# Kernel tuning notes

Measured on AMD Instinct MI355X. Metric: run time of the kernel, lower is better.

Reference implementation:

```python
import math
import jax, jax.numpy as jnp
import numpy as np

B, N, D = 4, 4096, 1024
H, M = 16, 64
HD = D // H  # 64
EPS = 1e-6


def favor_features(data, proj):
    # data: [B,H,N,hd], proj: [M,hd] -> [B,H,N,M]
    hd = data.shape[-1]
    m = proj.shape[0]
    dn = data / math.sqrt(hd)
    norm_sq = 0.5 * jnp.sum(dn * dn, axis=-1, keepdims=True)  # [B,H,N,1]
    comb = jnp.einsum('bhnd,md->bhnm', dn, proj) - norm_sq
    comb = comb - jnp.max(comb, axis=-1, keepdims=True)
    return jnp.exp(comb) / math.sqrt(m) + EPS


def setup_inputs() -> dict:
    key = jax.random.key(0)
    ks = jax.random.split(key, 6)
    x = jax.random.normal(ks[0], (B, N, D), dtype=jnp.float32)
    qkv_w = jax.random.normal(ks[1], (3 * D, D), dtype=jnp.float32) * (1.0 / math.sqrt(D))
    qkv_b = jnp.zeros((3 * D,), dtype=jnp.float32)
    proj_w = jax.random.normal(ks[2], (D, D), dtype=jnp.float32) * (1.0 / math.sqrt(D))
    proj_b = jnp.zeros((D,), dtype=jnp.float32)
    pm = jax.random.normal(ks[3], (M, HD), dtype=jnp.float32)
    pm = pm / jnp.linalg.norm(pm, axis=-1, keepdims=True)
    return {"x": x, "qkv_w": qkv_w, "qkv_b": qkv_b, "proj_w": proj_w,
            "proj_b": proj_b, "projection_matrix": pm}


def reference(x, qkv_w, qkv_b, proj_w, proj_b, projection_matrix):
    b, n, d = x.shape
    qkv = x @ qkv_w.T + qkv_b                      # [B,N,3D]
    qkv = qkv.reshape(b, n, 3, H, HD)
    qkv = jnp.transpose(qkv, (2, 0, 3, 1, 4))      # [3,B,H,N,hd]
    q, k, v = qkv[0], qkv[1], qkv[2]
    q_p = favor_features(q, projection_matrix)     # [B,H,N,M]
    k_p = favor_features(k, projection_matrix)     # [B,H,N,M]
    kv = jnp.einsum('bhnm,bhnv->bhmv', k_p, v)     # [B,H,M,hd]
    out = jnp.einsum('bhnm,bhmv->bhnv', q_p, kv)   # [B,H,N,hd]
    k_sum = jnp.sum(k_p, axis=2)                   # [B,H,M]
    normalizer = jnp.einsum('bhnm,bhm->bhn', q_p, k_sum)[..., None]
    out = out / (normalizer + EPS)
    out = jnp.transpose(out, (0, 2, 1, 3)).reshape(b, n, d)
    return out @ proj_w.T + proj_b
```

## Files before the change

kernel.cpp:

```cpp
#include <hip/hip_runtime.h>
#include <math.h>

#define B_  4
#define N_  4096
#define D_  1024
#define H_  16
#define HD_ 64
#define M_  64
#define TD_ 3072
#define EPS_ 1e-6f

typedef __attribute__((ext_vector_type(8))) short short8;
typedef __attribute__((ext_vector_type(4))) float floatx4;
typedef unsigned int uint32;
typedef unsigned short ushort;

__device__ __forceinline__ void cvt2(float f0, float f1, uint32& hp, uint32& lp)
{
    uint32 b0 = __float_as_uint(f0), b1 = __float_as_uint(f1);
    hp = (b1 & 0xFFFF0000u) | (b0 >> 16);
    float l0 = f0 - __uint_as_float(b0 & 0xFFFF0000u);
    float l1 = f1 - __uint_as_float(b1 & 0xFFFF0000u);
    lp = (__float_as_uint(l1) & 0xFFFF0000u) | (__float_as_uint(l0) >> 16);
}

__global__ __launch_bounds__(256) void split_kernel(
    const float* __restrict__ src, ushort* __restrict__ hi,
    ushort* __restrict__ lo, int n)
{
    size_t i = ((size_t)blockIdx.x * 256 + threadIdx.x) * 8;
    if (i >= (size_t)n) return;
    float4 f0 = *(const float4*)(src + i);
    float4 f1 = *(const float4*)(src + i + 4);
    uint4 h, l;
    cvt2(f0.x, f0.y, h.x, l.x); cvt2(f0.z, f0.w, h.y, l.y);
    cvt2(f1.x, f1.y, h.z, l.z); cvt2(f1.z, f1.w, h.w, l.w);
    *(uint4*)(hi + i) = h;
    *(uint4*)(lo + i) = l;
}

#define LDSTR 40

__global__ __launch_bounds__(256, 2) void gemm_presplit_nt_bias(
    const ushort* __restrict__ Ah, const ushort* __restrict__ Al,
    const ushort* __restrict__ Bh, const ushort* __restrict__ Bl,
    const float* __restrict__ bias, float* __restrict__ C,
    int Nx, int Kx)
{
    __shared__ __align__(16) ushort AhiS[128*LDSTR], AloS[128*LDSTR];
    __shared__ __align__(16) ushort BhiS[128*LDSTR], BloS[128*LDSTR];

    const int t    = threadIdx.x;
    const int bm   = blockIdx.y * 128, bn = blockIdx.x * 128;
    const int lane = t & 63, wave = t >> 6;
    const int wm   = wave >> 1, wn = wave & 1;
    const int l16  = lane & 15, quad = lane >> 4;
    const int r    = t >> 1;
    const int ko   = (t & 1) * 16;

    floatx4 acc[4][4];
#pragma unroll
    for (int i = 0; i < 4; i++)
#pragma unroll
        for (int j = 0; j < 4; j++) acc[i][j] = (floatx4)0.f;

    const ushort* aph = Ah + (size_t)(bm + r) * Kx + ko;
    const ushort* apl = Al + (size_t)(bm + r) * Kx + ko;
    const ushort* bph = Bh + (size_t)(bn + r) * Kx + ko;
    const ushort* bpl = Bl + (size_t)(bn + r) * Kx + ko;

    for (int k0 = 0; k0 < Kx; k0 += 32) {
        uint4 vah0 = *(const uint4*)(aph + k0);
        uint4 vah1 = *(const uint4*)(aph + k0 + 8);
        uint4 val0 = *(const uint4*)(apl + k0);
        uint4 val1 = *(const uint4*)(apl + k0 + 8);
        uint4 vbh0 = *(const uint4*)(bph + k0);
        uint4 vbh1 = *(const uint4*)(bph + k0 + 8);
        uint4 vbl0 = *(const uint4*)(bpl + k0);
        uint4 vbl1 = *(const uint4*)(bpl + k0 + 8);

        __syncthreads();

        *(uint4*)&AhiS[r*LDSTR + ko]     = vah0;
        *(uint4*)&AhiS[r*LDSTR + ko + 8] = vah1;
        *(uint4*)&AloS[r*LDSTR + ko]     = val0;
        *(uint4*)&AloS[r*LDSTR + ko + 8] = val1;
        *(uint4*)&BhiS[r*LDSTR + ko]     = vbh0;
        *(uint4*)&BhiS[r*LDSTR + ko + 8] = vbh1;
        *(uint4*)&BloS[r*LDSTR + ko]     = vbl0;
        *(uint4*)&BloS[r*LDSTR + ko + 8] = vbl1;

        __syncthreads();

        short8 ah[4], al[4], bh[4], bl[4];
#pragma unroll
        for (int mi = 0; mi < 4; mi++) {
            int row = (wm*64 + mi*16 + l16) * LDSTR + quad*8;
            ah[mi] = *(const short8*)&AhiS[row];
            al[mi] = *(const short8*)&AloS[row];
        }
#pragma unroll
        for (int ni = 0; ni < 4; ni++) {
            int row = (wn*64 + ni*16 + l16) * LDSTR + quad*8;
            bh[ni] = *(const short8*)&BhiS[row];
            bl[ni] = *(const short8*)&BloS[row];
        }
#pragma unroll
        for (int mi = 0; mi < 4; mi++)
#pragma unroll
            for (int ni = 0; ni < 4; ni++) {
                floatx4 d = acc[mi][ni];
                d = __builtin_amdgcn_mfma_f32_16x16x32_bf16(ah[mi], bh[ni], d, 0, 0, 0);
                d = __builtin_amdgcn_mfma_f32_16x16x32_bf16(al[mi], bh[ni], d, 0, 0, 0);
                d = __builtin_amdgcn_mfma_f32_16x16x32_bf16(ah[mi], bl[ni], d, 0, 0, 0);
                acc[mi][ni] = d;
            }
    }

    float bia[4];
#pragma unroll
    for (int ni = 0; ni < 4; ni++)
        bia[ni] = bias[bn + wn*64 + ni*16 + l16];
#pragma unroll
    for (int mi = 0; mi < 4; mi++)
#pragma unroll
        for (int rr = 0; rr < 4; rr++) {
            int row = bm + wm*64 + mi*16 + quad*4 + rr;
            float* crow = C + (size_t)row * Nx + bn + wn*64 + l16;
#pragma unroll
            for (int ni = 0; ni < 4; ni++)
                crow[ni*16] = acc[mi][ni][rr] + bia[ni];
        }
}

__device__ __forceinline__ void gload16(const void* g, void* l)
{
    __builtin_amdgcn_global_load_lds(
        (const __attribute__((address_space(1))) unsigned int*)g,
        (__attribute__((address_space(3))) unsigned int*)l,
        16, 0, 0);
}

#define BAR() asm volatile("s_barrier" ::: "memory")

__global__ __launch_bounds__(512, 2) void gemm256_pipe(
    const ushort* __restrict__ Ah, const ushort* __restrict__ Al,
    const ushort* __restrict__ Bh, const ushort* __restrict__ Bl,
    const float* __restrict__ bias, float* __restrict__ C,
    int Nx, int Kx)
{
    __shared__ __align__(16) ushort lds[65536];

    const int t    = threadIdx.x;
    const int wave = t >> 6, lane = t & 63;
    const int wm   = wave >> 2, wn = wave & 3;
    const int l16  = lane & 15, quad = lane >> 4;

    const int gx  = gridDim.x;
    const int nwg = gx * gridDim.y;
    int bid = blockIdx.y * gx + blockIdx.x;
    const int cpx = nwg >> 3;
    bid = (bid & 7) * cpx + (bid >> 3);
    const int bm = (bid / gx) * 256;
    const int bn = (bid % gx) * 256;

    const int r0   = t >> 2;
    const int cswz = ((((t & 3) << 4) ^ ((t & 0x18) << 1)) >> 1);
    const size_t aOff = (size_t)(bm + r0) * Kx + cswz;
    const size_t bOff = (size_t)(bn + r0) * Kx + cswz;

    const int ucol = (quad * 8) ^ ((l16 & 6) << 2);
    const int aRB  = (wm * 64 + l16) * 32 + ucol;
    const int bRB  = (wn * 32 + l16) * 32 + ucol;

    floatx4 acc[8][4];
#pragma unroll
    for (int i = 0; i < 8; i++)
#pragma unroll
        for (int j = 0; j < 4; j++) acc[i][j] = (floatx4)0.f;

#define STAGE_A2(NB, KT) do {                                                 \
    size_t g0_ = (size_t)(KT) * 32;                                           \
    gload16(Ah + aOff + g0_,                   &lds[(NB) + wave*512]);        \
    gload16(Al + aOff + g0_,                   &lds[(NB) + 8192 + wave*512]); \
    gload16(Ah + aOff + (size_t)128*Kx + g0_,  &lds[(NB) + 4096 + wave*512]); \
    gload16(Al + aOff + (size_t)128*Kx + g0_,  &lds[(NB) + 12288 + wave*512]);\
} while (0)
#define STAGE_B2(NB, KT) do {                                                 \
    size_t g0_ = (size_t)(KT) * 32;                                           \
    gload16(Bh + bOff + g0_,                   &lds[(NB) + 16384 + wave*512]);\
    gload16(Bl + bOff + g0_,                   &lds[(NB) + 24576 + wave*512]);\
    gload16(Bh + bOff + (size_t)128*Kx + g0_,  &lds[(NB) + 20480 + wave*512]);\
    gload16(Bl + bOff + (size_t)128*Kx + g0_,  &lds[(NB) + 28672 + wave*512]);\
} while (0)

    const int NT = Kx >> 5;

    STAGE_A2(0, 0);
    STAGE_B2(0, 0);
    asm volatile("s_waitcnt vmcnt(0)" ::: "memory");
    BAR();

    for (int kt = 0; kt < NT; kt++) {
        const int cb  = (kt & 1) << 15;
        const int nb  = cb ^ 32768;
        const int ktn = (kt + 1 < NT) ? kt + 1 : NT - 1;

        short8 ah_[4], al_[4], bh_[4], bl_[4];
        const int aB0 = cb + aRB;
        const int bB0 = cb + 16384 + bRB;

        STAGE_A2(nb, ktn);

#pragma unroll
        for (int g = 0; g < 4; g++) {
            bh_[g] = *(const short8*)&lds[bB0 + (g >> 1)*4096 + (g & 1)*512];
            bl_[g] = *(const short8*)&lds[bB0 + 8192 + (g >> 1)*4096 + (g & 1)*512];
        }
#pragma unroll
        for (int mi = 0; mi < 4; mi++) {
            ah_[mi] = *(const short8*)&lds[aB0 + mi*512];
            al_[mi] = *(const short8*)&lds[aB0 + 8192 + mi*512];
        }
        asm volatile("s_waitcnt lgkmcnt(0)" ::: "memory");
        __builtin_amdgcn_sched_barrier(0);
        __builtin_amdgcn_s_setprio(1);
#pragma unroll
        for (int mi = 0; mi < 4; mi++)
#pragma unroll
            for (int g = 0; g < 4; g++) {
                floatx4 d = acc[mi][g];
                d = __builtin_amdgcn_mfma_f32_16x16x32_bf16(ah_[mi], bh_[g], d, 0, 0, 0);
                d = __builtin_amdgcn_mfma_f32_16x16x32_bf16(al_[mi], bh_[g], d, 0, 0, 0);
                d = __builtin_amdgcn_mfma_f32_16x16x32_bf16(ah_[mi], bl_[g], d, 0, 0, 0);
                acc[mi][g] = d;
            }
        __builtin_amdgcn_s_setprio(0);
        __builtin_amdgcn_sched_barrier(0);

        STAGE_B2(nb, ktn);
#pragma unroll
        for (int mi = 0; mi < 4; mi++) {
            ah_[mi] = *(const short8*)&lds[aB0 + 4096 + mi*512];
            al_[mi] = *(const short8*)&lds[aB0 + 12288 + mi*512];
        }
        asm volatile("s_waitcnt lgkmcnt(0)" ::: "memory");
        __builtin_amdgcn_sched_barrier(0);
        __builtin_amdgcn_s_setprio(1);
#pragma unroll
        for (int mi = 0; mi < 4; mi++)
#pragma unroll
            for (int g = 0; g < 4; g++) {
                floatx4 d = acc[4 + mi][g];
                d = __builtin_amdgcn_mfma_f32_16x16x32_bf16(ah_[mi], bh_[g], d, 0, 0, 0);
                d = __builtin_amdgcn_mfma_f32_16x16x32_bf16(al_[mi], bh_[g], d, 0, 0, 0);
                d = __builtin_amdgcn_mfma_f32_16x16x32_bf16(ah_[mi], bl_[g], d, 0, 0, 0);
                acc[4 + mi][g] = d;
            }
        __builtin_amdgcn_s_setprio(0);
        __builtin_amdgcn_sched_barrier(0);

        asm volatile("s_waitcnt vmcnt(0)" ::: "memory");
        BAR();
    }

#pragma unroll
    for (int f = 0; f < 8; f++) {
        const int row = bm + (f >> 2)*128 + wm*64 + (f & 3)*16 + quad*4;
#pragma unroll
        for (int g = 0; g < 4; g++) {
            const int col = bn + (g >> 1)*128 + wn*32 + (g & 1)*16 + l16;
            const float bb = bias[col];
#pragma unroll
            for (int rr = 0; rr < 4; rr++)
                C[(size_t)(row + rr) * Nx + col] = acc[f][g][rr] + bb;
        }
    }
#undef STAGE_A2
#undef STAGE_B2
}

__global__ __launch_bounds__(256) void favor_features_kernel(
    const float* __restrict__ qkvb, const float* __restrict__ proj,
    float* __restrict__ qp, float* __restrict__ kp)
{
    __shared__ float  projT[64*64];
    __shared__ float4 dnbuf[4][64];
    const int t = threadIdx.x;
    const int wave = t >> 6, lane = t & 63;
    const int part = blockIdx.y;
    float* outp = (part == 0) ? qp : kp;

    for (int i = t; i < 4096; i += 256)
        projT[(i & 63) * 64 + (i >> 6)] = proj[i];
    __syncthreads();

    const int h = blockIdx.x >> 6;
    const int n0 = (blockIdx.x & 63) * 64;
    const float* src = qkvb + part * D_ + h * HD_ + lane;

    for (int iter = 0; iter < 4; iter++) {
        const int n = n0 + iter * 16 + wave * 4;
        float v0 = src[(size_t)(n+0) * TD_];
        float v1 = src[(size_t)(n+1) * TD_];
        float v2 = src[(size_t)(n+2) * TD_];
        float v3 = src[(size_t)(n+3) * TD_];
        float4 dn = make_float4(v0*0.125f, v1*0.125f, v2*0.125f, v3*0.125f);
        dnbuf[wave][lane] = dn;
        float s0 = dn.x*dn.x, s1 = dn.y*dn.y, s2 = dn.z*dn.z, s3 = dn.w*dn.w;
#pragma unroll
        for (int off = 32; off >= 1; off >>= 1) {
            s0 += __shfl_xor(s0, off, 64);
            s1 += __shfl_xor(s1, off, 64);
            s2 += __shfl_xor(s2, off, 64);
            s3 += __shfl_xor(s3, off, 64);
        }
        float c0 = -0.5f*s0, c1 = -0.5f*s1, c2 = -0.5f*s2, c3 = -0.5f*s3;
#pragma unroll
        for (int d = 0; d < 64; d++) {
            float p = projT[d*64 + lane];
            float4 q = dnbuf[wave][d];
            c0 = fmaf(q.x, p, c0);
            c1 = fmaf(q.y, p, c1);
            c2 = fmaf(q.z, p, c2);
            c3 = fmaf(q.w, p, c3);
        }
        float m0 = c0, m1 = c1, m2 = c2, m3 = c3;
#pragma unroll
        for (int off = 32; off >= 1; off >>= 1) {
            m0 = fmaxf(m0, __shfl_xor(m0, off, 64));
            m1 = fmaxf(m1, __shfl_xor(m1, off, 64));
            m2 = fmaxf(m2, __shfl_xor(m2, off, 64));
            m3 = fmaxf(m3, __shfl_xor(m3, off, 64));
        }
        float r0 = expf(c0 - m0) * 0.125f + EPS_;
        float r1 = expf(c1 - m1) * 0.125f + EPS_;
        float r2 = expf(c2 - m2) * 0.125f + EPS_;
        float r3 = expf(c3 - m3) * 0.125f + EPS_;
        size_t orow = ((size_t)h * N_ + n) * 64 + lane;
        outp[orow]       = r0;
        outp[orow + 64]  = r1;
        outp[orow + 128] = r2;
        outp[orow + 192] = r3;
    }
}

__global__ __launch_bounds__(256) void kv_partial_kernel(
    const float* __restrict__ qkvb, const float* __restrict__ kp,
    float* __restrict__ kvpart, float* __restrict__ kspart)
{
    const int t = threadIdx.x;
    const int h = blockIdx.x;
    const int c = blockIdx.y;
    const int n0 = c * 128;
    const int m0 = (t & 15) * 4;
    const int v0 = (t >> 4) * 4;

    const float* kpsrc = kp + ((size_t)h * N_ + n0) * 64 + m0;
    const float* vsrc  = qkvb + (size_t)n0 * TD_ + 2 * D_ + h * HD_ + v0;

    float acc[4][4];
#pragma unroll
    for (int i = 0; i < 4; i++)
#pragma unroll
        for (int j = 0; j < 4; j++) acc[i][j] = 0.f;
    float ks[4] = {0.f, 0.f, 0.f, 0.f};

#pragma unroll 4
    for (int n = 0; n < 128; n++) {
        float4 kq = *(const float4*)(kpsrc + (size_t)n * 64);
        float4 vq = *(const float4*)(vsrc  + (size_t)n * TD_);
        acc[0][0] = fmaf(kq.x, vq.x, acc[0][0]);
        acc[0][1] = fmaf(kq.x, vq.y, acc[0][1]);
        acc[0][2] = fmaf(kq.x, vq.z, acc[0][2]);
        acc[0][3] = fmaf(kq.x, vq.w, acc[0][3]);
        acc[1][0] = fmaf(kq.y, vq.x, acc[1][0]);
        acc[1][1] = fmaf(kq.y, vq.y, acc[1][1]);
        acc[1][2] = fmaf(kq.y, vq.z, acc[1][2]);
        acc[1][3] = fmaf(kq.y, vq.w, acc[1][3]);
        acc[2][0] = fmaf(kq.z, vq.x, acc[2][0]);
        acc[2][1] = fmaf(kq.z, vq.y, acc[2][1]);
        acc[2][2] = fmaf(kq.z, vq.z, acc[2][2]);
        acc[2][3] = fmaf(kq.z, vq.w, acc[2][3]);
        acc[3][0] = fmaf(kq.w, vq.x, acc[3][0]);
        acc[3][1] = fmaf(kq.w, vq.y, acc[3][1]);
        acc[3][2] = fmaf(kq.w, vq.z, acc[3][2]);
        acc[3][3] = fmaf(kq.w, vq.w, acc[3][3]);
        if (v0 == 0) {
            ks[0] += kq.x; ks[1] += kq.y; ks[2] += kq.z; ks[3] += kq.w;
        }
    }

    float* kvp = kvpart + (((size_t)h * 32 + c) * 4096) + m0 * 64 + v0;
#pragma unroll
    for (int i = 0; i < 4; i++)
        *(float4*)(kvp + i * 64) = make_float4(acc[i][0], acc[i][1], acc[i][2], acc[i][3]);

    if (v0 == 0) {
        float* ksp = kspart + ((size_t)h * 32 + c) * 64 + m0;
        *(float4*)ksp = make_float4(ks[0], ks[1], ks[2], ks[3]);
    }
}

__global__ __launch_bounds__(256) void kv_reduce_kernel(
    const float* __restrict__ kvpart, const float* __restrict__ kspart,
    float* __restrict__ kv, float* __restrict__ ksum)
{
    const int t = threadIdx.x;
    const int h = blockIdx.x;
    const int e0 = t * 16;

    float4 s[4];
#pragma unroll
    for (int i = 0; i < 4; i++) s[i] = make_float4(0.f, 0.f, 0.f, 0.f);
    float kss = 0.f;

    for (int c = 0; c < 32; c++) {
        const float* p = kvpart + (((size_t)h * 32 + c) * 4096) + e0;
#pragma unroll
        for (int i = 0; i < 4; i++) {
            float4 x = *(const float4*)(p + i * 4);
            s[i].x += x.x; s[i].y += x.y; s[i].z += x.z; s[i].w += x.w;
        }
        if (t < 64) kss += kspart[((size_t)h * 32 + c) * 64 + t];
    }

    float* kvo = kv + (size_t)h * 4096 + e0;
#pragma unroll
    for (int i = 0; i < 4; i++) *(float4*)(kvo + i * 4) = s[i];
    if (t < 64) ksum[h * 64 + t] = kss;
}

__global__ __launch_bounds__(256) void out_kernel(
    const float* __restrict__ qp, const float* __restrict__ kv,
    const float* __restrict__ ksum, ushort* __restrict__ attn_hi,
    ushort* __restrict__ attn_lo)
{
    __shared__ float  kvs[4096];
    __shared__ float  kss[64];
    __shared__ float4 qbuf[4][64];
    const int t = threadIdx.x, lane = t & 63, wave = t >> 6;
    const int h = blockIdx.x;
    const int n0 = blockIdx.y * 64;

    for (int i = t; i < 4096; i += 256) kvs[i] = kv[(size_t)h * 4096 + i];
    if (t < 64) kss[t] = ksum[h * 64 + t];
    __syncthreads();

    const float* qsrc = qp + (size_t)h * N_ * 64 + lane;
    const size_t dbase = h * HD_ + lane;

    for (int iter = 0; iter < 4; iter++) {
        const int n = n0 + iter * 16 + wave * 4;
        float q0 = qsrc[(size_t)(n+0) * 64];
        float q1 = qsrc[(size_t)(n+1) * 64];
        float q2 = qsrc[(size_t)(n+2) * 64];
        float q3 = qsrc[(size_t)(n+3) * 64];
        qbuf[wave][lane] = make_float4(q0, q1, q2, q3);
        float t0 = q0 * kss[lane], t1 = q1 * kss[lane];
        float t2 = q2 * kss[lane], t3 = q3 * kss[lane];
#pragma unroll
        for (int off = 32; off >= 1; off >>= 1) {
            t0 += __shfl_xor(t0, off, 64);
            t1 += __shfl_xor(t1, off, 64);
            t2 += __shfl_xor(t2, off, 64);
            t3 += __shfl_xor(t3, off, 64);
        }
        float a0 = 0.f, a1 = 0.f, a2 = 0.f, a3 = 0.f;
#pragma unroll
        for (int m = 0; m < 64; m++) {
            float kvv = kvs[m*64 + lane];
            float4 q = qbuf[wave][m];
            a0 = fmaf(q.x, kvv, a0);
            a1 = fmaf(q.y, kvv, a1);
            a2 = fmaf(q.z, kvv, a2);
            a3 = fmaf(q.w, kvv, a3);
        }
        float r[4];
        r[0] = a0 / (t0 + EPS_); r[1] = a1 / (t1 + EPS_);
        r[2] = a2 / (t2 + EPS_); r[3] = a3 / (t3 + EPS_);
#pragma unroll
        for (int i = 0; i < 4; i++) {
            uint32 bits = __float_as_uint(r[i]);
            float lof = r[i] - __uint_as_float(bits & 0xFFFF0000u);
            size_t idx = (size_t)(n + i) * D_ + dbase;
            attn_hi[idx] = (ushort)(bits >> 16);
            attn_lo[idx] = (ushort)(__float_as_uint(lof) >> 16);
        }
    }
}

extern "C" void kernel_launch(void* const* d_in, const int* in_sizes, int n_in,
                              void* d_out, int out_size, void* d_ws, size_t ws_size,
                              hipStream_t stream)
{
    const float* x      = (const float*)d_in[0];
    const float* qkv_w  = (const float*)d_in[1];
    const float* qkv_b  = (const float*)d_in[2];
    const float* proj_w = (const float*)d_in[3];
    const float* proj_b = (const float*)d_in[4];
    const float* pm     = (const float*)d_in[5];
    float* out = (float*)d_out;
    float* ws  = (float*)d_ws;

    const bool tierA = ws_size >= 327553024ULL;
    const bool tierB = ws_size >= 176558080ULL;

    if (tierA) {
        float* qkvbA  = ws;
        float* qp     = qkvbA + 50331648;
        float* kp     = qp + 4194304;
        float* kvb    = kp + 4194304;
        float* ksum   = kvb + 65536;
        float* kvpart = ksum + 1024;
        float* kspart = kvpart + 2097152;
        float* axw    = kspart + 32768;
        float* wsplit = axw + 16777216;

        ushort* xw_hi    = (ushort*)axw;
        ushort* xw_lo    = xw_hi + 16777216;
        ushort* attn_hi  = xw_hi;
        ushort* attn_lo  = xw_lo;
        ushort* qkvw_hi  = (ushort*)wsplit;
        ushort* qkvw_lo  = qkvw_hi + 3145728;
        ushort* projw_hi = qkvw_lo + 3145728;
        ushort* projw_lo = projw_hi + 1048576;

        split_kernel<<<1536, 256, 0, stream>>>(qkv_w, qkvw_hi, qkvw_lo, TD_*D_);
        split_kernel<<<512,  256, 0, stream>>>(proj_w, projw_hi, projw_lo, D_*D_);
        split_kernel<<<8192, 256, 0, stream>>>(x, xw_hi, xw_lo, B_*N_*D_);

        gemm256_pipe<<<dim3(12, 64), 512, 0, stream>>>(
            xw_hi, xw_lo, qkvw_hi, qkvw_lo, qkv_b, qkvbA, TD_, D_);

        for (int b = 0; b < B_; b++) {
            const float* qkvb = qkvbA + (size_t)b * N_ * TD_;
            dim3 g2(1024, 2);
            favor_features_kernel<<<g2, 256, 0, stream>>>(qkvb, pm, qp, kp);
            dim3 g3(16, 32);
            kv_partial_kernel<<<g3, 256, 0, stream>>>(qkvb, kp, kvpart, kspart);
            kv_reduce_kernel<<<16, 256, 0, stream>>>(kvpart, kspart, kvb, ksum);
            dim3 g4(16, 64);
            out_kernel<<<g4, 256, 0, stream>>>(qp, kvb, ksum,
                attn_hi + (size_t)b * N_ * D_, attn_lo + (size_t)b * N_ * D_);
        }

        gemm256_pipe<<<dim3(4, 64), 512, 0, stream>>>(
            attn_hi, attn_lo, projw_hi, projw_lo, proj_b, out, D_, D_);
    } else if (tierB) {
        float* qkvb   = ws;
        float* qp     = ws + 12582912;
        float* kp     = qp + 4194304;
        float* kvb    = kp + 4194304;
        float* ksum   = kvb + 65536;
        float* kvpart = ksum + 1024;
        float* kspart = kvpart + 2097152;
        float* wsplit = kspart + 32768;
        float* attnA  = wsplit + 4194304;

        ushort* xw_hi    = (ushort*)qp;
        ushort* xw_lo    = xw_hi + 4194304;
        ushort* qkvw_hi  = (ushort*)wsplit;
        ushort* qkvw_lo  = qkvw_hi + 3145728;
        ushort* projw_hi = qkvw_lo + 3145728;
        ushort* projw_lo = projw_hi + 1048576;
        ushort* attnA_hi = (ushort*)attnA;
        ushort* attnA_lo = attnA_hi + 16777216;

        split_kernel<<<1536, 256, 0, stream>>>(qkv_w, qkvw_hi, qkvw_lo, TD_*D_);
        split_kernel<<<512,  256, 0, stream>>>(proj_w, projw_hi, projw_lo, D_*D_);

        for (int b = 0; b < B_; b++) {
            const float* xb = x + (size_t)b * N_ * D_;
            split_kernel<<<2048, 256, 0, stream>>>(xb, xw_hi, xw_lo, N_*D_);
            gemm256_pipe<<<dim3(12, 16), 512, 0, stream>>>(
                xw_hi, xw_lo, qkvw_hi, qkvw_lo, qkv_b, qkvb, TD_, D_);
            dim3 g2(1024, 2);
            favor_features_kernel<<<g2, 256, 0, stream>>>(qkvb, pm, qp, kp);
            dim3 g3(16, 32);
            kv_partial_kernel<<<g3, 256, 0, stream>>>(qkvb, kp, kvpart, kspart);
            kv_reduce_kernel<<<16, 256, 0, stream>>>(kvpart, kspart, kvb, ksum);
            dim3 g4(16, 64);
            out_kernel<<<g4, 256, 0, stream>>>(qp, kvb, ksum,
                attnA_hi + (size_t)b * N_ * D_, attnA_lo + (size_t)b * N_ * D_);
        }

        gemm256_pipe<<<dim3(4, 64), 512, 0, stream>>>(
            attnA_hi, attnA_lo, projw_hi, projw_lo, proj_b, out, D_, D_);
    } else {
        float* qkvb   = ws;
        float* qpreg  = ws + 12582912;
        float* kpreg  = qpreg + 4194304;
        float* kvb    = kpreg + 4194304;
        float* ksum   = kvb + 65536;
        float* kvpart = ksum + 1024;
        float* kspart = kvpart + 2097152;
        float* wsplit = kspart + 32768;

        ushort* xw_hi   = (ushort*)qpreg;
        ushort* xw_lo   = xw_hi + 4194304;
        float*  qp      = qpreg;
        float*  kp      = kpreg;
        ushort* attn_hi = (ushort*)kpreg;
        ushort* attn_lo = attn_hi + 4194304;
        ushort* qkvw_hi = (ushort*)wsplit;
        ushort* qkvw_lo = qkvw_hi + 3145728;
        ushort* projw_hi= qkvw_lo + 3145728;
        ushort* projw_lo= projw_hi + 1048576;

        split_kernel<<<TD_*D_/2048, 256, 0, stream>>>(qkv_w, qkvw_hi, qkvw_lo, TD_*D_);
        split_kernel<<<D_*D_/2048,  256, 0, stream>>>(proj_w, projw_hi, projw_lo, D_*D_);

        for (int b = 0; b < B_; b++) {
            const float* xb = x + (size_t)b * N_ * D_;
            float* outb = out + (size_t)b * N_ * D_;

            split_kernel<<<N_*D_/2048, 256, 0, stream>>>(xb, xw_hi, xw_lo, N_*D_);

            gemm256_pipe<<<dim3(12, 16), 512, 0, stream>>>(
                xw_hi, xw_lo, qkvw_hi, qkvw_lo, qkv_b, qkvb, TD_, D_);

            dim3 g2(1024, 2);
            favor_features_kernel<<<g2, 256, 0, stream>>>(qkvb, pm, qp, kp);

            dim3 g3(16, 32);
            kv_partial_kernel<<<g3, 256, 0, stream>>>(qkvb, kp, kvpart, kspart);
            kv_reduce_kernel<<<16, 256, 0, stream>>>(kvpart, kspart, kvb, ksum);

            dim3 g4(16, 64);
            out_kernel<<<g4, 256, 0, stream>>>(qp, kvb, ksum, attn_hi, attn_lo);

            dim3 g5(D_ / 128, N_ / 128);
            gemm_presplit_nt_bias<<<g5, 256, 0, stream>>>(
                attn_hi, attn_lo, projw_hi, projw_lo, proj_b, outb, D_, D_);
        }
    }
}
```

Before: 965.0 us.

## Issue both GEMM stage loads early and widen kv_reduce grid

In the pipelined GEMM main loop, the B-tile prefetch is now issued together with the A-tile prefetch at the top of each iteration. The explicit lgkmcnt waits and sched_barriers around the MFMA blocks are removed, leaving the compiler to schedule LDS reads and MFMAs. Separately, kv_reduce is split across 4x more blocks, each thread summing one float4 instead of four, to raise parallelism in a tiny kernel. Removing the manual waits and barriers risks worse instruction interleaving or extra register pressure.

```diff
diff --git a/kernel.cpp b/kernel.cpp
--- a/kernel.cpp
+++ b/kernel.cpp
@@ -141,7 +141,7 @@
         16, 0, 0);
 }
 
-#define BAR() asm volatile("s_barrier" ::: "memory")
+#define BAR()  asm volatile("s_barrier" ::: "memory")
 
 __global__ __launch_bounds__(512, 2) void gemm256_pipe(
     const ushort* __restrict__ Ah, const ushort* __restrict__ Al,
@@ -211,6 +211,7 @@
         const int bB0 = cb + 16384 + bRB;
 
         STAGE_A2(nb, ktn);
+        STAGE_B2(nb, ktn);
 
 #pragma unroll
         for (int g = 0; g < 4; g++) {
@@ -222,8 +223,6 @@
             ah_[mi] = *(const short8*)&lds[aB0 + mi*512];
             al_[mi] = *(const short8*)&lds[aB0 + 8192 + mi*512];
         }
-        asm volatile("s_waitcnt lgkmcnt(0)" ::: "memory");
-        __builtin_amdgcn_sched_barrier(0);
         __builtin_amdgcn_s_setprio(1);
 #pragma unroll
         for (int mi = 0; mi < 4; mi++)
@@ -236,16 +235,12 @@
                 acc[mi][g] = d;
             }
         __builtin_amdgcn_s_setprio(0);
-        __builtin_amdgcn_sched_barrier(0);
-
-        STAGE_B2(nb, ktn);
+
 #pragma unroll
         for (int mi = 0; mi < 4; mi++) {
             ah_[mi] = *(const short8*)&lds[aB0 + 4096 + mi*512];
             al_[mi] = *(const short8*)&lds[aB0 + 12288 + mi*512];
         }
-        asm volatile("s_waitcnt lgkmcnt(0)" ::: "memory");
-        __builtin_amdgcn_sched_barrier(0);
         __builtin_amdgcn_s_setprio(1);
 #pragma unroll
         for (int mi = 0; mi < 4; mi++)
@@ -258,7 +253,6 @@
                 acc[4 + mi][g] = d;
             }
         __builtin_amdgcn_s_setprio(0);
-        __builtin_amdgcn_sched_barrier(0);
 
         asm volatile("s_waitcnt vmcnt(0)" ::: "memory");
         BAR();
@@ -408,27 +402,20 @@
 {
     const int t = threadIdx.x;
     const int h = blockIdx.x;
-    const int e0 = t * 16;
-
-    float4 s[4];
-#pragma unroll
-    for (int i = 0; i < 4; i++) s[i] = make_float4(0.f, 0.f, 0.f, 0.f);
+    const int e0 = (blockIdx.y * 256 + t) * 4;
+
+    float4 s = make_float4(0.f, 0.f, 0.f, 0.f);
     float kss = 0.f;
+    const bool doks = (blockIdx.y == 0) && (t < 64);
 
     for (int c = 0; c < 32; c++) {
-        const float* p = kvpart + (((size_t)h * 32 + c) * 4096) + e0;
-#pragma unroll
-        for (int i = 0; i < 4; i++) {
-            float4 x = *(const float4*)(p + i * 4);
-            s[i].x += x.x; s[i].y += x.y; s[i].z += x.z; s[i].w += x.w;
-        }
-        if (t < 64) kss += kspart[((size_t)h * 32 + c) * 64 + t];
-    }
-
-    float* kvo = kv + (size_t)h * 4096 + e0;
-#pragma unroll
-    for (int i = 0; i < 4; i++) *(float4*)(kvo + i * 4) = s[i];
-    if (t < 64) ksum[h * 64 + t] = kss;
+        float4 x = *(const float4*)(kvpart + (((size_t)h * 32 + c) * 4096) + e0);
+        s.x += x.x; s.y += x.y; s.z += x.z; s.w += x.w;
+        if (doks) kss += kspart[((size_t)h * 32 + c) * 64 + t];
+    }
+
+    *(float4*)(kv + (size_t)h * 4096 + e0) = s;
+    if (doks) ksum[h * 64 + t] = kss;
 }
 
 __global__ __launch_bounds__(256) void out_kernel(
@@ -539,7 +526,7 @@
             favor_features_kernel<<<g2, 256, 0, stream>>>(qkvb, pm, qp, kp);
             dim3 g3(16, 32);
             kv_partial_kernel<<<g3, 256, 0, stream>>>(qkvb, kp, kvpart, kspart);
-            kv_reduce_kernel<<<16, 256, 0, stream>>>(kvpart, kspart, kvb, ksum);
+            kv_reduce_kernel<<<dim3(16, 4), 256, 0, stream>>>(kvpart, kspart, kvb, ksum);
             dim3 g4(16, 64);
             out_kernel<<<g4, 256, 0, stream>>>(qp, kvb, ksum,
                 attn_hi + (size_t)b * N_ * D_, attn_lo + (size_t)b * N_ * D_);
@@ -579,7 +566,7 @@
             favor_features_kernel<<<g2, 256, 0, stream>>>(qkvb, pm, qp, kp);
             dim3 g3(16, 32);
             kv_partial_kernel<<<g3, 256, 0, stream>>>(qkvb, kp, kvpart, kspart);
-            kv_reduce_kernel<<<16, 256, 0, stream>>>(kvpart, kspart, kvb, ksum);
+            kv_reduce_kernel<<<dim3(16, 4), 256, 0, stream>>>(kvpart, kspart, kvb, ksum);
             dim3 g4(16, 64);
             out_kernel<<<g4, 256, 0, stream>>>(qp, kvb, ksum,
                 attnA_hi + (size_t)b * N_ * D_, attnA_lo + (size_t)b * N_ * D_);
@@ -625,7 +612,7 @@
 
             dim3 g3(16, 32);
             kv_partial_kernel<<<g3, 256, 0, stream>>>(qkvb, kp, kvpart, kspart);
-            kv_reduce_kernel<<<16, 256, 0, stream>>>(kvpart, kspart, kvb, ksum);
+            kv_reduce_kernel<<<dim3(16, 4), 256, 0, stream>>>(kvpart, kspart, kvb, ksum);
 
             dim3 g4(16, 64);
             out_kernel<<<g4, 256, 0, stream>>>(qp, kvb, ksum, attn_hi, attn_lo);
```

Result: no change. 949.1 us (-1.6%).
